# Kernel tuning notes

Measured on AMD Instinct MI355X. Metric: run time of the kernel, lower is better.

## Reference

```python
import jax, jax.numpy as jnp
import numpy as np

T, K, E, H, I = 1024, 2, 8, 2048, 1024


def setup_inputs() -> dict:
    key = jax.random.key(0)
    k1, k2, k3, k4 = jax.random.split(key, 4)
    hidden_states = jax.random.normal(k1, (T, H), dtype=jnp.float32)
    selected_experts = jax.random.randint(k2, (T, K), 0, E, dtype=jnp.int32)
    # glorot-ish scale for the batched expert kernels
    gu_scale = (2.0 / (H + 2 * I)) ** 0.5
    dn_scale = (2.0 / (I + H)) ** 0.5
    gate_up_proj = jax.random.normal(k3, (E, 2 * I, H), dtype=jnp.float32) * gu_scale
    down_proj = jax.random.normal(k4, (E, H, I), dtype=jnp.float32) * dn_scale
    return {
        "hidden_states": hidden_states,
        "selected_experts": selected_experts,
        "gate_up_proj": gate_up_proj,
        "down_proj": down_proj,
    }


def reference(hidden_states, selected_experts, gate_up_proj, down_proj):
    # Mathematically identical to the original per-token weight gather
    # (ops.take + 'th,temh->tem'), but expressed as dense all-expert GEMMs
    # followed by an output gather, avoiding the T*k*2I*H weight blowup.
    # gate_up_all: (T, E, 2I)
    gate_up_all = jnp.einsum("th,emh->tem", hidden_states, gate_up_proj)
    gate, up = jnp.split(gate_up_all, 2, axis=-1)
    intermediate = jax.nn.silu(gate) * up                # (T, E, I)
    out_all = jnp.einsum("tem,ehm->teh", intermediate, down_proj)  # (T, E, H)
    # select the top-k experts' outputs per token -> (T, K, H)
    return jnp.take_along_axis(out_all, selected_experts[..., None].astype(jnp.int32), axis=1)
```

## Files before the change

kernel.cpp:

```cpp
#include <hip/hip_runtime.h>
#include <hip/hip_bf16.h>

#define T_TOK 1024
#define KSEL  2
#define NEXP  8
#define HDIM  2048
#define IDIM  1024
#define TK    2048

#define BR 72
#define MT 3

typedef float  f32x4  __attribute__((ext_vector_type(4)));
typedef __bf16 bf16x8 __attribute__((ext_vector_type(8)));
typedef __bf16 bf16x2 __attribute__((ext_vector_type(2)));

__device__ __forceinline__ unsigned short f2bf(float f) {
    union { float f; unsigned u; } v; v.f = f;
    unsigned r = (v.u >> 16) & 1u;
    return (unsigned short)((v.u + 0x7fffu + r) >> 16);
}

__device__ __forceinline__ unsigned pk2bf(float lo, float hi) {
#if __has_builtin(__builtin_amdgcn_cvt_pk_bf16_f32)
    bf16x2 v = __builtin_amdgcn_cvt_pk_bf16_f32(lo, hi);
    union { bf16x2 v; unsigned u; } c; c.v = v;
    return c.u;
#else
    return (unsigned)f2bf(lo) | ((unsigned)f2bf(hi) << 16);
#endif
}

__global__ __launch_bounds__(256) void prep(
    const float* __restrict__ hidden, const int* __restrict__ sel,
    unsigned short* __restrict__ hid_bf, int* __restrict__ meta,
    int* __restrict__ pairs)
{
    const int t = blockIdx.x * 256 + threadIdx.x;
    {
        const float* s = hidden + (size_t)t * 8;
        float4 v0 = *(const float4*)s;
        float4 v1 = *(const float4*)(s + 4);
        uint4 o;
        o.x = pk2bf(v0.x, v0.y); o.y = pk2bf(v0.z, v0.w);
        o.z = pk2bf(v1.x, v1.y); o.w = pk2bf(v1.z, v1.w);
        *(uint4*)(hid_bf + (size_t)t * 8) = o;
    }
    if (blockIdx.x == 0) {
        __shared__ int lcnt[NEXP], lstart[NEXP], lfill[NEXP];
        const int tid = threadIdx.x;
        if (tid < NEXP) { lcnt[tid] = 0; lfill[tid] = 0; }
        __syncthreads();
        for (int i = tid; i < TK; i += 256) atomicAdd(&lcnt[sel[i]], 1);
        __syncthreads();
        if (tid == 0) {
            int s2 = 0;
            for (int e2 = 0; e2 < NEXP; ++e2) { lstart[e2] = s2; s2 += lcnt[e2]; }
        }
        __syncthreads();
        for (int i = tid; i < TK; i += 256) {
            int e2 = sel[i];
            pairs[lstart[e2] + atomicAdd(&lfill[e2], 1)] = i;
        }
        if (tid < NEXP) { meta[tid] = lcnt[tid]; meta[NEXP + tid] = lstart[tid]; }
    }
}

__global__ __launch_bounds__(512, 2) void gemm1_gateup(
    const unsigned short* __restrict__ hid_bf, const float* __restrict__ gup,
    const int* __restrict__ meta, const int* __restrict__ pairs,
    unsigned short* __restrict__ inter)
{
    __shared__ __align__(16) unsigned short Bs[3][64 * BR];

    const int bx = blockIdx.x;
    const int e = bx & 7, nt = (bx >> 3) & 31, mt = bx >> 8;
    const int cnt = meta[e];
    const int m0 = mt * 384;
    if (m0 >= cnt) return;
    const int seg  = meta[8 + e];
    const int rows = cnt - m0;
    const int n0   = nt * 32;

    const int tid  = threadIdx.x;
    const int lane = tid & 63, w = tid >> 6;
    const int quad = lane >> 4, l16 = lane & 15;

    const int brow = tid >> 3, bkc = (tid & 7) * 8;
    const int grow = (brow < 32) ? (n0 + brow) : (IDIM + n0 + (brow - 32));
    const float* __restrict__ bp =
        gup + (size_t)e * (2 * IDIM * HDIM) + (size_t)grow * HDIM + bkc;
    const int bofs = brow * BR + bkc;

    const unsigned short* ap[3];
    #pragma unroll
    for (int i = 0; i < 3; ++i) {
        int mr  = m0 + w * 48 + i * 16 + l16;
        int idx = seg + min(mr, cnt - 1);
        ap[i] = hid_bf + (size_t)(pairs[idx] >> 1) * HDIM + quad * 8;
    }

    f32x4 accg[3][2], accu[3][2];
    const f32x4 zero = {0.f, 0.f, 0.f, 0.f};
    #pragma unroll
    for (int i = 0; i < 3; ++i)
        #pragma unroll
        for (int j = 0; j < 2; ++j) { accg[i][j] = zero; accu[i][j] = zero; }

    float4 Br0[2], Br1[2];
    bf16x8 afA[3][2], afB[3][2];

    auto loadB = [&](float4 (&br)[2], int s) {
        const float* p = bp + s * 64;
        br[0] = *(const float4*)p;
        br[1] = *(const float4*)(p + 4);
    };
    auto storeB = [&](const float4 (&br)[2], int buf) {
        uint4 o;
        o.x = pk2bf(br[0].x, br[0].y); o.y = pk2bf(br[0].z, br[0].w);
        o.z = pk2bf(br[1].x, br[1].y); o.w = pk2bf(br[1].z, br[1].w);
        *(uint4*)&Bs[buf][bofs] = o;
    };
    auto loadA = [&](bf16x8 (&af)[3][2], int s) {
        #pragma unroll
        for (int i = 0; i < 3; ++i)
            #pragma unroll
            for (int kk = 0; kk < 2; ++kk)
                af[i][kk] = *(const bf16x8*)(ap[i] + s * 64 + kk * 32);
    };
    auto compute = [&](const bf16x8 (&af)[3][2], int buf) {
        #pragma unroll
        for (int kk = 0; kk < 2; ++kk) {
            const int ko = kk * 32 + quad * 8;
            bf16x8 bg[2], bu[2];
            #pragma unroll
            for (int j = 0; j < 2; ++j) {
                bg[j] = *(const bf16x8*)&Bs[buf][(j * 16 + l16) * BR + ko];
                bu[j] = *(const bf16x8*)&Bs[buf][(32 + j * 16 + l16) * BR + ko];
            }
            #pragma unroll
            for (int i = 0; i < 3; ++i)
                #pragma unroll
                for (int j = 0; j < 2; ++j) {
                    accg[i][j] = __builtin_amdgcn_mfma_f32_16x16x32_bf16(af[i][kk], bg[j], accg[i][j], 0, 0, 0);
                    accu[i][j] = __builtin_amdgcn_mfma_f32_16x16x32_bf16(af[i][kk], bu[j], accu[i][j], 0, 0, 0);
                }
        }
    };

    const int NK = HDIM / 64;
    loadB(Br0, 0);
    loadA(afA, 0);
    storeB(Br0, 0);
    loadB(Br0, 1);
    loadB(Br1, 2);
    __syncthreads();

    for (int s = 0; s < NK; s += 2) {
        storeB(Br0, (s + 1) % 3);
        if (s + 3 < NK) loadB(Br0, s + 3);
        loadA(afB, s + 1);
        compute(afA, s % 3);
        __syncthreads();
        if (s + 2 < NK) storeB(Br1, (s + 2) % 3);
        if (s + 4 < NK) loadB(Br1, s + 4);
        if (s + 2 < NK) loadA(afA, s + 2);
        compute(afB, (s + 1) % 3);
        __syncthreads();
    }

    #pragma unroll
    for (int i = 0; i < 3; ++i) {
        #pragma unroll
        for (int r = 0; r < 4; ++r) {
            int mrow = w * 48 + i * 16 + quad * 4 + r;
            if (mrow < rows && mrow < 384) {
                size_t orow = (size_t)(seg + m0 + mrow) * IDIM;
                #pragma unroll
                for (int j = 0; j < 2; ++j) {
                    float g = accg[i][j][r], u = accu[i][j][r];
                    float sv = g * (1.f / (1.f + __expf(-g)));
                    inter[orow + n0 + j * 16 + l16] = f2bf(sv * u);
                }
            }
        }
    }
}

__global__ __launch_bounds__(512, 2) void gemm2_down(
    const unsigned short* __restrict__ inter, const float* __restrict__ down,
    const int* __restrict__ meta, const int* __restrict__ pairs,
    float* __restrict__ out)
{
    __shared__ __align__(16) unsigned short Bs[3][64 * BR];

    const int bx = blockIdx.x;
    const int e = bx & 7, nt = (bx >> 3) & 31, mt = bx >> 8;
    const int cnt = meta[e];
    const int m0 = mt * 384;
    if (m0 >= cnt) return;
    const int seg  = meta[8 + e];
    const int rows = cnt - m0;
    const int n0   = nt * 64;

    const int tid  = threadIdx.x;
    const int lane = tid & 63, w = tid >> 6;
    const int quad = lane >> 4, l16 = lane & 15;

    const int brow = tid >> 3, bkc = (tid & 7) * 8;
    const float* __restrict__ bp =
        down + (size_t)e * (HDIM * IDIM) + (size_t)(n0 + brow) * IDIM + bkc;
    const int bofs = brow * BR + bkc;

    const unsigned short* ap[3];
    #pragma unroll
    for (int i = 0; i < 3; ++i) {
        int mr  = m0 + w * 48 + i * 16 + l16;
        int idx = seg + min(mr, cnt - 1);
        ap[i] = inter + (size_t)idx * IDIM + quad * 8;
    }

    f32x4 acc[3][4];
    const f32x4 zero = {0.f, 0.f, 0.f, 0.f};
    #pragma unroll
    for (int i = 0; i < 3; ++i)
        #pragma unroll
        for (int j = 0; j < 4; ++j) acc[i][j] = zero;

    float4 Br0[2], Br1[2];
    bf16x8 afA[3][2], afB[3][2];

    auto loadB = [&](float4 (&br)[2], int s) {
        const float* p = bp + s * 64;
        br[0] = *(const float4*)p;
        br[1] = *(const float4*)(p + 4);
    };
    auto storeB = [&](const float4 (&br)[2], int buf) {
        uint4 o;
        o.x = pk2bf(br[0].x, br[0].y); o.y = pk2bf(br[0].z, br[0].w);
        o.z = pk2bf(br[1].x, br[1].y); o.w = pk2bf(br[1].z, br[1].w);
        *(uint4*)&Bs[buf][bofs] = o;
    };
    auto loadA = [&](bf16x8 (&af)[3][2], int s) {
        #pragma unroll
        for (int i = 0; i < 3; ++i)
            #pragma unroll
            for (int kk = 0; kk < 2; ++kk)
                af[i][kk] = *(const bf16x8*)(ap[i] + s * 64 + kk * 32);
    };
    auto compute = [&](const bf16x8 (&af)[3][2], int buf) {
        #pragma unroll
        for (int kk = 0; kk < 2; ++kk) {
            const int ko = kk * 32 + quad * 8;
            bf16x8 bf[4];
            #pragma unroll
            for (int j = 0; j < 4; ++j)
                bf[j] = *(const bf16x8*)&Bs[buf][(j * 16 + l16) * BR + ko];
            #pragma unroll
            for (int i = 0; i < 3; ++i)
                #pragma unroll
                for (int j = 0; j < 4; ++j)
                    acc[i][j] = __builtin_amdgcn_mfma_f32_16x16x32_bf16(af[i][kk], bf[j], acc[i][j], 0, 0, 0);
        }
    };

    const int NK = IDIM / 64;
    loadB(Br0, 0);
    loadA(afA, 0);
    storeB(Br0, 0);
    loadB(Br0, 1);
    loadB(Br1, 2);
    __syncthreads();

    for (int s = 0; s < NK; s += 2) {
        storeB(Br0, (s + 1) % 3);
        if (s + 3 < NK) loadB(Br0, s + 3);
        loadA(afB, s + 1);
        compute(afA, s % 3);
        __syncthreads();
        if (s + 2 < NK) storeB(Br1, (s + 2) % 3);
        if (s + 4 < NK) loadB(Br1, s + 4);
        if (s + 2 < NK) loadA(afA, s + 2);
        compute(afB, (s + 1) % 3);
        __syncthreads();
    }

    #pragma unroll
    for (int i = 0; i < 3; ++i) {
        #pragma unroll
        for (int r = 0; r < 4; ++r) {
            int mrow = w * 48 + i * 16 + quad * 4 + r;
            if (mrow < rows && mrow < 384) {
                int p = pairs[seg + m0 + mrow];
                size_t ob = (size_t)p * HDIM + n0 + l16;
                #pragma unroll
                for (int j = 0; j < 4; ++j)
                    out[ob + j * 16] = acc[i][j][r];
            }
        }
    }
}

extern "C" void kernel_launch(void* const* d_in, const int* in_sizes, int n_in,
                              void* d_out, int out_size, void* d_ws, size_t ws_size,
                              hipStream_t stream) {
    const float* hidden = (const float*)d_in[0];
    const int*   sel    = (const int*)  d_in[1];
    const float* gup    = (const float*)d_in[2];
    const float* down   = (const float*)d_in[3];
    float* out = (float*)d_out;

    char* ws = (char*)d_ws;
    int* meta  = (int*)ws;
    int* pairs = meta + 16;
    unsigned short* inter  = (unsigned short*)(ws + 16384);
    unsigned short* hid_bf = inter + (size_t)TK * IDIM;

    prep<<<T_TOK * HDIM / 8 / 256, 256, 0, stream>>>(hidden, sel, hid_bf, meta, pairs);
    gemm1_gateup<<<MT * 32 * 8, 512, 0, stream>>>(hid_bf, gup, meta, pairs, inter);
    gemm2_down  <<<MT * 32 * 8, 512, 0, stream>>>(inter, down, meta, pairs, out);
}
```

Baseline: 285.6 us.

## Load expert weights directly into MFMA registers per wave, dropping LDS staging

Both expert GEMMs no longer stage fp32 weight tiles through shared memory with block-wide barriers. Each wave now independently owns a 64-row by 16-column (gate/up) or 32-column (down) output tile, loads its B operands straight from global memory in MFMA fragment layout, and converts them to bf16 in registers. Blocks shrink to 256 threads and the grid is remapped so waves index (m-tile, n-tile) pairs per expert. This removes LDS traffic and synchronisation, but weight rows are re-read by every m-tile wave, so reuse now depends on L2 hits, and per-lane global loads are less coalesced.

```diff
diff --git a/kernel.cpp b/kernel.cpp
--- a/kernel.cpp
+++ b/kernel.cpp
@@ -7,9 +7,6 @@
 #define HDIM  2048
 #define IDIM  1024
 #define TK    2048
-
-#define BR 72
-#define MT 3
 
 typedef float  f32x4  __attribute__((ext_vector_type(4)));
 typedef __bf16 bf16x8 __attribute__((ext_vector_type(8)));
@@ -29,6 +26,13 @@
 #else
     return (unsigned)f2bf(lo) | ((unsigned)f2bf(hi) << 16);
 #endif
+}
+
+__device__ __forceinline__ bf16x8 cvt8(float4 a, float4 b) {
+    union { unsigned u[4]; bf16x8 v; } c;
+    c.u[0] = pk2bf(a.x, a.y); c.u[1] = pk2bf(a.z, a.w);
+    c.u[2] = pk2bf(b.x, b.y); c.u[3] = pk2bf(b.z, b.w);
+    return c.v;
 }
 
 __global__ __launch_bounds__(256) void prep(
@@ -66,236 +70,191 @@
     }
 }
 
-__global__ __launch_bounds__(512, 2) void gemm1_gateup(
+__global__ __launch_bounds__(256, 2) void gemm1_gateup(
     const unsigned short* __restrict__ hid_bf, const float* __restrict__ gup,
     const int* __restrict__ meta, const int* __restrict__ pairs,
     unsigned short* __restrict__ inter)
 {
-    __shared__ __align__(16) unsigned short Bs[3][64 * BR];
-
     const int bx = blockIdx.x;
-    const int e = bx & 7, nt = (bx >> 3) & 31, mt = bx >> 8;
-    const int cnt = meta[e];
-    const int m0 = mt * 384;
-    if (m0 >= cnt) return;
-    const int seg  = meta[8 + e];
-    const int rows = cnt - m0;
-    const int n0   = nt * 32;
-
-    const int tid  = threadIdx.x;
+    const int e = bx & 7;
+    const int tid = threadIdx.x;
     const int lane = tid & 63, w = tid >> 6;
     const int quad = lane >> 4, l16 = lane & 15;
-
-    const int brow = tid >> 3, bkc = (tid & 7) * 8;
-    const int grow = (brow < 32) ? (n0 + brow) : (IDIM + n0 + (brow - 32));
-    const float* __restrict__ bp =
-        gup + (size_t)e * (2 * IDIM * HDIM) + (size_t)grow * HDIM + bkc;
-    const int bofs = brow * BR + bkc;
-
-    const unsigned short* ap[3];
-    #pragma unroll
-    for (int i = 0; i < 3; ++i) {
-        int mr  = m0 + w * 48 + i * 16 + l16;
+    const int widx = (bx >> 3) * 4 + w;
+    const int nt = widx / 6, mi = widx - nt * 6;
+    const int cnt = meta[e];
+    const int m0 = mi * 64;
+    if (m0 >= cnt) return;
+    const int seg = meta[8 + e];
+    const int n0 = nt * 16;
+
+    const unsigned short* ap[4];
+    #pragma unroll
+    for (int i = 0; i < 4; ++i) {
+        int mr  = m0 + i * 16 + l16;
         int idx = seg + min(mr, cnt - 1);
         ap[i] = hid_bf + (size_t)(pairs[idx] >> 1) * HDIM + quad * 8;
     }
-
-    f32x4 accg[3][2], accu[3][2];
+    const float* __restrict__ bpg =
+        gup + (size_t)e * (2 * IDIM * HDIM) + (size_t)(n0 + l16) * HDIM + quad * 8;
+    const float* __restrict__ bpu =
+        gup + (size_t)e * (2 * IDIM * HDIM) + (size_t)(IDIM + n0 + l16) * HDIM + quad * 8;
+
+    f32x4 accg[4], accu[4];
     const f32x4 zero = {0.f, 0.f, 0.f, 0.f};
     #pragma unroll
-    for (int i = 0; i < 3; ++i)
-        #pragma unroll
-        for (int j = 0; j < 2; ++j) { accg[i][j] = zero; accu[i][j] = zero; }
-
-    float4 Br0[2], Br1[2];
-    bf16x8 afA[3][2], afB[3][2];
-
-    auto loadB = [&](float4 (&br)[2], int s) {
-        const float* p = bp + s * 64;
-        br[0] = *(const float4*)p;
-        br[1] = *(const float4*)(p + 4);
-    };
-    auto storeB = [&](const float4 (&br)[2], int buf) {
-        uint4 o;
-        o.x = pk2bf(br[0].x, br[0].y); o.y = pk2bf(br[0].z, br[0].w);
-        o.z = pk2bf(br[1].x, br[1].y); o.w = pk2bf(br[1].z, br[1].w);
-        *(uint4*)&Bs[buf][bofs] = o;
-    };
-    auto loadA = [&](bf16x8 (&af)[3][2], int s) {
-        #pragma unroll
-        for (int i = 0; i < 3; ++i)
+    for (int i = 0; i < 4; ++i) { accg[i] = zero; accu[i] = zero; }
+
+    float4 Rg0[2][2], Ru0[2][2], Rg1[2][2], Ru1[2][2];
+    bf16x8 afA[4][2], afB[4][2];
+
+    auto loadB = [&](float4 (&Rg)[2][2], float4 (&Ru)[2][2], int s) {
+        #pragma unroll
+        for (int kk = 0; kk < 2; ++kk) {
+            const int o = s * 64 + kk * 32;
+            Rg[kk][0] = *(const float4*)(bpg + o);
+            Rg[kk][1] = *(const float4*)(bpg + o + 4);
+            Ru[kk][0] = *(const float4*)(bpu + o);
+            Ru[kk][1] = *(const float4*)(bpu + o + 4);
+        }
+    };
+    auto loadA = [&](bf16x8 (&af)[4][2], int s) {
+        #pragma unroll
+        for (int i = 0; i < 4; ++i)
             #pragma unroll
             for (int kk = 0; kk < 2; ++kk)
                 af[i][kk] = *(const bf16x8*)(ap[i] + s * 64 + kk * 32);
     };
-    auto compute = [&](const bf16x8 (&af)[3][2], int buf) {
-        #pragma unroll
-        for (int kk = 0; kk < 2; ++kk) {
-            const int ko = kk * 32 + quad * 8;
-            bf16x8 bg[2], bu[2];
-            #pragma unroll
-            for (int j = 0; j < 2; ++j) {
-                bg[j] = *(const bf16x8*)&Bs[buf][(j * 16 + l16) * BR + ko];
-                bu[j] = *(const bf16x8*)&Bs[buf][(32 + j * 16 + l16) * BR + ko];
-            }
-            #pragma unroll
-            for (int i = 0; i < 3; ++i)
-                #pragma unroll
-                for (int j = 0; j < 2; ++j) {
-                    accg[i][j] = __builtin_amdgcn_mfma_f32_16x16x32_bf16(af[i][kk], bg[j], accg[i][j], 0, 0, 0);
-                    accu[i][j] = __builtin_amdgcn_mfma_f32_16x16x32_bf16(af[i][kk], bu[j], accu[i][j], 0, 0, 0);
-                }
+    auto compute = [&](const bf16x8 (&af)[4][2],
+                       const float4 (&Rg)[2][2], const float4 (&Ru)[2][2]) {
+        #pragma unroll
+        for (int kk = 0; kk < 2; ++kk) {
+            bf16x8 bg = cvt8(Rg[kk][0], Rg[kk][1]);
+            bf16x8 bu = cvt8(Ru[kk][0], Ru[kk][1]);
+            #pragma unroll
+            for (int i = 0; i < 4; ++i) {
+                accg[i] = __builtin_amdgcn_mfma_f32_16x16x32_bf16(af[i][kk], bg, accg[i], 0, 0, 0);
+                accu[i] = __builtin_amdgcn_mfma_f32_16x16x32_bf16(af[i][kk], bu, accu[i], 0, 0, 0);
+            }
         }
     };
 
     const int NK = HDIM / 64;
-    loadB(Br0, 0);
+    loadB(Rg0, Ru0, 0);
     loadA(afA, 0);
-    storeB(Br0, 0);
-    loadB(Br0, 1);
-    loadB(Br1, 2);
-    __syncthreads();
-
+    loadB(Rg1, Ru1, 1);
     for (int s = 0; s < NK; s += 2) {
-        storeB(Br0, (s + 1) % 3);
-        if (s + 3 < NK) loadB(Br0, s + 3);
         loadA(afB, s + 1);
-        compute(afA, s % 3);
-        __syncthreads();
-        if (s + 2 < NK) storeB(Br1, (s + 2) % 3);
-        if (s + 4 < NK) loadB(Br1, s + 4);
-        if (s + 2 < NK) loadA(afA, s + 2);
-        compute(afB, (s + 1) % 3);
-        __syncthreads();
-    }
-
-    #pragma unroll
-    for (int i = 0; i < 3; ++i) {
+        compute(afA, Rg0, Ru0);
+        if (s + 2 < NK) { loadB(Rg0, Ru0, s + 2); loadA(afA, s + 2); }
+        compute(afB, Rg1, Ru1);
+        if (s + 3 < NK) loadB(Rg1, Ru1, s + 3);
+    }
+
+    #pragma unroll
+    for (int i = 0; i < 4; ++i) {
         #pragma unroll
         for (int r = 0; r < 4; ++r) {
-            int mrow = w * 48 + i * 16 + quad * 4 + r;
-            if (mrow < rows && mrow < 384) {
-                size_t orow = (size_t)(seg + m0 + mrow) * IDIM;
-                #pragma unroll
-                for (int j = 0; j < 2; ++j) {
-                    float g = accg[i][j][r], u = accu[i][j][r];
-                    float sv = g * (1.f / (1.f + __expf(-g)));
-                    inter[orow + n0 + j * 16 + l16] = f2bf(sv * u);
-                }
-            }
-        }
-    }
-}
-
-__global__ __launch_bounds__(512, 2) void gemm2_down(
+            int mrow = m0 + i * 16 + quad * 4 + r;
+            if (mrow < cnt) {
+                float g = accg[i][r], u = accu[i][r];
+                float sv = g * (1.f / (1.f + __expf(-g)));
+                inter[(size_t)(seg + mrow) * IDIM + n0 + l16] = f2bf(sv * u);
+            }
+        }
+    }
+}
+
+__global__ __launch_bounds__(256, 2) void gemm2_down(
     const unsigned short* __restrict__ inter, const float* __restrict__ down,
     const int* __restrict__ meta, const int* __restrict__ pairs,
     float* __restrict__ out)
 {
-    __shared__ __align__(16) unsigned short Bs[3][64 * BR];
-
     const int bx = blockIdx.x;
-    const int e = bx & 7, nt = (bx >> 3) & 31, mt = bx >> 8;
-    const int cnt = meta[e];
-    const int m0 = mt * 384;
-    if (m0 >= cnt) return;
-    const int seg  = meta[8 + e];
-    const int rows = cnt - m0;
-    const int n0   = nt * 64;
-
-    const int tid  = threadIdx.x;
+    const int e = bx & 7;
+    const int tid = threadIdx.x;
     const int lane = tid & 63, w = tid >> 6;
     const int quad = lane >> 4, l16 = lane & 15;
-
-    const int brow = tid >> 3, bkc = (tid & 7) * 8;
-    const float* __restrict__ bp =
-        down + (size_t)e * (HDIM * IDIM) + (size_t)(n0 + brow) * IDIM + bkc;
-    const int bofs = brow * BR + bkc;
-
-    const unsigned short* ap[3];
-    #pragma unroll
-    for (int i = 0; i < 3; ++i) {
-        int mr  = m0 + w * 48 + i * 16 + l16;
+    const int widx = (bx >> 3) * 4 + w;
+    const int nt = widx / 6, mi = widx - nt * 6;
+    const int cnt = meta[e];
+    const int m0 = mi * 64;
+    if (m0 >= cnt) return;
+    const int seg = meta[8 + e];
+    const int n0 = nt * 32;
+
+    const unsigned short* ap[4];
+    #pragma unroll
+    for (int i = 0; i < 4; ++i) {
+        int mr  = m0 + i * 16 + l16;
         int idx = seg + min(mr, cnt - 1);
         ap[i] = inter + (size_t)idx * IDIM + quad * 8;
     }
-
-    f32x4 acc[3][4];
+    const float* __restrict__ bp0 =
+        down + (size_t)e * (HDIM * IDIM) + (size_t)(n0 + l16) * IDIM + quad * 8;
+    const float* __restrict__ bp1 =
+        down + (size_t)e * (HDIM * IDIM) + (size_t)(n0 + 16 + l16) * IDIM + quad * 8;
+
+    f32x4 acc[4][2];
     const f32x4 zero = {0.f, 0.f, 0.f, 0.f};
     #pragma unroll
-    for (int i = 0; i < 3; ++i)
-        #pragma unroll
-        for (int j = 0; j < 4; ++j) acc[i][j] = zero;
-
-    float4 Br0[2], Br1[2];
-    bf16x8 afA[3][2], afB[3][2];
-
-    auto loadB = [&](float4 (&br)[2], int s) {
-        const float* p = bp + s * 64;
-        br[0] = *(const float4*)p;
-        br[1] = *(const float4*)(p + 4);
-    };
-    auto storeB = [&](const float4 (&br)[2], int buf) {
-        uint4 o;
-        o.x = pk2bf(br[0].x, br[0].y); o.y = pk2bf(br[0].z, br[0].w);
-        o.z = pk2bf(br[1].x, br[1].y); o.w = pk2bf(br[1].z, br[1].w);
-        *(uint4*)&Bs[buf][bofs] = o;
-    };
-    auto loadA = [&](bf16x8 (&af)[3][2], int s) {
-        #pragma unroll
-        for (int i = 0; i < 3; ++i)
+    for (int i = 0; i < 4; ++i) { acc[i][0] = zero; acc[i][1] = zero; }
+
+    float4 R0[2][2][2], R1[2][2][2];
+    bf16x8 afA[4][2], afB[4][2];
+
+    auto loadB = [&](float4 (&R)[2][2][2], int s) {
+        #pragma unroll
+        for (int kk = 0; kk < 2; ++kk) {
+            const int o = s * 64 + kk * 32;
+            R[kk][0][0] = *(const float4*)(bp0 + o);
+            R[kk][0][1] = *(const float4*)(bp0 + o + 4);
+            R[kk][1][0] = *(const float4*)(bp1 + o);
+            R[kk][1][1] = *(const float4*)(bp1 + o + 4);
+        }
+    };
+    auto loadA = [&](bf16x8 (&af)[4][2], int s) {
+        #pragma unroll
+        for (int i = 0; i < 4; ++i)
             #pragma unroll
             for (int kk = 0; kk < 2; ++kk)
                 af[i][kk] = *(const bf16x8*)(ap[i] + s * 64 + kk * 32);
     };
-    auto compute = [&](const bf16x8 (&af)[3][2], int buf) {
-        #pragma unroll
-        for (int kk = 0; kk < 2; ++kk) {
-            const int ko = kk * 32 + quad * 8;
-            bf16x8 bf[4];
-            #pragma unroll
-            for (int j = 0; j < 4; ++j)
-                bf[j] = *(const bf16x8*)&Bs[buf][(j * 16 + l16) * BR + ko];
-            #pragma unroll
-            for (int i = 0; i < 3; ++i)
-                #pragma unroll
-                for (int j = 0; j < 4; ++j)
-                    acc[i][j] = __builtin_amdgcn_mfma_f32_16x16x32_bf16(af[i][kk], bf[j], acc[i][j], 0, 0, 0);
+    auto compute = [&](const bf16x8 (&af)[4][2], const float4 (&R)[2][2][2]) {
+        #pragma unroll
+        for (int kk = 0; kk < 2; ++kk) {
+            bf16x8 b0 = cvt8(R[kk][0][0], R[kk][0][1]);
+            bf16x8 b1 = cvt8(R[kk][1][0], R[kk][1][1]);
+            #pragma unroll
+            for (int i = 0; i < 4; ++i) {
+                acc[i][0] = __builtin_amdgcn_mfma_f32_16x16x32_bf16(af[i][kk], b0, acc[i][0], 0, 0, 0);
+                acc[i][1] = __builtin_amdgcn_mfma_f32_16x16x32_bf16(af[i][kk], b1, acc[i][1], 0, 0, 0);
+            }
         }
     };
 
     const int NK = IDIM / 64;
-    loadB(Br0, 0);
+    loadB(R0, 0);
     loadA(afA, 0);
-    storeB(Br0, 0);
-    loadB(Br0, 1);
-    loadB(Br1, 2);
-    __syncthreads();
-
+    loadB(R1, 1);
     for (int s = 0; s < NK; s += 2) {
-        storeB(Br0, (s + 1) % 3);
-        if (s + 3 < NK) loadB(Br0, s + 3);
         loadA(afB, s + 1);
-        compute(afA, s % 3);
-        __syncthreads();
-        if (s + 2 < NK) storeB(Br1, (s + 2) % 3);
-        if (s + 4 < NK) loadB(Br1, s + 4);
-        if (s + 2 < NK) loadA(afA, s + 2);
-        compute(afB, (s + 1) % 3);
-        __syncthreads();
-    }
-
-    #pragma unroll
-    for (int i = 0; i < 3; ++i) {
+        compute(afA, R0);
+        if (s + 2 < NK) { loadB(R0, s + 2); loadA(afA, s + 2); }
+        compute(afB, R1);
+        if (s + 3 < NK) loadB(R1, s + 3);
+    }
+
+    #pragma unroll
+    for (int i = 0; i < 4; ++i) {
         #pragma unroll
         for (int r = 0; r < 4; ++r) {
-            int mrow = w * 48 + i * 16 + quad * 4 + r;
-            if (mrow < rows && mrow < 384) {
-                int p = pairs[seg + m0 + mrow];
+            int mrow = m0 + i * 16 + quad * 4 + r;
+            if (mrow < cnt) {
+                int p = pairs[seg + mrow];
                 size_t ob = (size_t)p * HDIM + n0 + l16;
-                #pragma unroll
-                for (int j = 0; j < 4; ++j)
-                    out[ob + j * 16] = acc[i][j][r];
+                out[ob]      = acc[i][0][r];
+                out[ob + 16] = acc[i][1][r];
             }
         }
     }
@@ -317,6 +276,6 @@
     unsigned short* hid_bf = inter + (size_t)TK * IDIM;
 
     prep<<<T_TOK * HDIM / 8 / 256, 256, 0, stream>>>(hidden, sel, hid_bf, meta, pairs);
-    gemm1_gateup<<<MT * 32 * 8, 512, 0, stream>>>(hid_bf, gup, meta, pairs, inter);
-    gemm2_down  <<<MT * 32 * 8, 512, 0, stream>>>(inter, down, meta, pairs, out);
-}
+    gemm1_gateup<<<8 * 96, 256, 0, stream>>>(hid_bf, gup, meta, pairs, inter);
+    gemm2_down  <<<8 * 96, 256, 0, stream>>>(inter, down, meta, pairs, out);
+}
```

Result: slower. 458.7 us (+60.6%).
